# Kernel optimization log

Hardware: AMD Instinct MI355X
Metric: run time of the kernel (lower is better)

The kernel has to match this reference:

```python
import jax, jax.numpy as jnp
import numpy as np
from jax.ops import segment_sum


def gcn_conv(x, edge_index, W, b):
    """PyG GCNConv: add self-loops, symmetric D^-1/2 (A+I) D^-1/2 normalization,
    then aggregate normalized messages at target nodes. edge_weight=None -> ones."""
    N = x.shape[0]
    loops = jnp.arange(N, dtype=edge_index.dtype)
    row = jnp.concatenate([edge_index[0], loops])  # source nodes
    col = jnp.concatenate([edge_index[1], loops])  # target nodes
    w = jnp.ones(row.shape[0], dtype=x.dtype)
    deg = segment_sum(w, col, num_segments=N)
    dinv = jnp.where(deg > 0, jax.lax.rsqrt(deg), 0.0)
    norm = dinv[row] * dinv[col]                    # [E+N]
    xw = x @ W                                      # dense transform [N, out]
    msg = xw[row] * norm[:, None]                   # gather + scale [E+N, out]
    out = segment_sum(msg, col, num_segments=N)     # scatter-add at targets
    return out + b


def setup_inputs() -> dict:
    key = jax.random.key(0)
    k1, k2, k3, k4 = jax.random.split(key, 4)
    N, E, nhid, nfeat = 50000, 800000, 256, 128
    x = jax.random.normal(k1, (N, nhid), dtype=jnp.float32)
    edge_index = jax.random.randint(k2, (2, E), 0, N, dtype=jnp.int64)
    W1 = jax.random.normal(k3, (nhid, nhid), dtype=jnp.float32) * (1.0 / np.sqrt(nhid))
    b1 = jnp.zeros((nhid,), dtype=jnp.float32)
    W2 = jax.random.normal(k4, (nhid, nfeat), dtype=jnp.float32) * (1.0 / np.sqrt(nhid))
    b2 = jnp.zeros((nfeat,), dtype=jnp.float32)
    return {"x": x, "edge_index": edge_index, "W1": W1, "b1": b1, "W2": W2, "b2": b2}


def reference(x, edge_index, W1, b1, W2, b2):
    h = jax.nn.relu(gcn_conv(x, edge_index, W1, b1))
    # dropout is identity in eval mode (deterministic reference)
    return gcn_conv(h, edge_index, W2, b2)
```

## Files before the change

kernel.cpp:

```cpp
#include <hip/hip_runtime.h>
#include <math.h>


typedef _Float16 h8 __attribute__((ext_vector_type(8)));
typedef float    f32x4 __attribute__((ext_vector_type(4)));

#define CAP 64

__global__ void k_zero(int* __restrict__ deg, int* __restrict__ govf, int N) {
    int i = blockIdx.x * blockDim.x + threadIdx.x;
    if (i < N) deg[i] = 0;
    if (i == 0) *govf = 0;
}

__global__ __launch_bounds__(256) void k_count_prep(
    const int* __restrict__ col, int E, int* __restrict__ deg, int* __restrict__ rank,
    int ncb,
    const float* __restrict__ W1, const float* __restrict__ W2,
    _Float16* __restrict__ wt1, _Float16* __restrict__ wt2,
    int K, int n1, int n2)
{
    if ((int)blockIdx.x < ncb) {
        int i = blockIdx.x * blockDim.x + threadIdx.x;
        int s = ncb * blockDim.x;
        for (int e = i; e < E; e += s) rank[e] = atomicAdd(&deg[col[e]], 1);
        return;
    }
    int i = (blockIdx.x - ncb) * blockDim.x + threadIdx.x;
    int c1 = K * n1;
    if (i < c1) {
        int k = i / n1, n = i % n1;
        wt1[(long)n * K + k] = (_Float16)W1[i];
    } else if (i < c1 + K * n2) {
        int j = i - c1;
        int k = j / n2, n = j % n2;
        wt2[(long)n * K + k] = (_Float16)W2[j];
    }
}

__device__ __forceinline__ void gemm1_body(
    const float* __restrict__ X32, const _Float16* __restrict__ Wt,
    _Float16* __restrict__ Y, int M, int K, int by)
{
    __shared__ _Float16 As[128][40];
    __shared__ _Float16 Bs[256][40];

    const int bm = by * 128;
    const int tid = threadIdx.x;
    const int w = tid >> 6, l = tid & 63;
    const int wm = (w >> 2) * 64, wn = (w & 3) * 64;
    const int lr = l & 15, lg = l >> 4;

    const int arow = tid >> 2, acol = (tid & 3) * 8;
    const int brow = tid >> 1, bcol = (tid & 1) * 16;

    f32x4 acc[4][4];
    #pragma unroll
    for (int i = 0; i < 4; i++)
        #pragma unroll
        for (int j = 0; j < 4; j++)
            acc[i][j] = (f32x4){0.f, 0.f, 0.f, 0.f};

    float4 pf0, pf1;
    h8 pb0, pb1;

    auto loadA = [&](int k0) {
        int gm = bm + arow; if (gm >= M) gm = M - 1;
        pf0 = *reinterpret_cast<const float4*>(&X32[(long)gm * K + k0 + acol]);
        pf1 = *reinterpret_cast<const float4*>(&X32[(long)gm * K + k0 + acol + 4]);
    };
    auto loadB = [&](int k0) {
        pb0 = *reinterpret_cast<const h8*>(&Wt[(long)brow * K + k0 + bcol]);
        pb1 = *reinterpret_cast<const h8*>(&Wt[(long)brow * K + k0 + bcol + 8]);
    };

    loadA(0); loadB(0);
    for (int k0 = 0; k0 < K; k0 += 32) {
        h8 hv;
        hv[0] = (_Float16)pf0.x; hv[1] = (_Float16)pf0.y;
        hv[2] = (_Float16)pf0.z; hv[3] = (_Float16)pf0.w;
        hv[4] = (_Float16)pf1.x; hv[5] = (_Float16)pf1.y;
        hv[6] = (_Float16)pf1.z; hv[7] = (_Float16)pf1.w;
        *reinterpret_cast<h8*>(&As[arow][acol]) = hv;
        *reinterpret_cast<h8*>(&Bs[brow][bcol]) = pb0;
        *reinterpret_cast<h8*>(&Bs[brow][bcol + 8]) = pb1;
        __syncthreads();

        if (k0 + 32 < K) { loadA(k0 + 32); loadB(k0 + 32); }

        h8 a[4], b[4];
        #pragma unroll
        for (int i = 0; i < 4; i++)
            a[i] = *reinterpret_cast<const h8*>(&As[wm + i * 16 + lr][lg * 8]);
        #pragma unroll
        for (int j = 0; j < 4; j++)
            b[j] = *reinterpret_cast<const h8*>(&Bs[wn + j * 16 + lr][lg * 8]);
        #pragma unroll
        for (int i = 0; i < 4; i++)
            #pragma unroll
            for (int j = 0; j < 4; j++)
                acc[i][j] = __builtin_amdgcn_mfma_f32_16x16x32_f16(
                    a[i], b[j], acc[i][j], 0, 0, 0);
        __syncthreads();
    }

    #pragma unroll
    for (int i = 0; i < 4; i++) {
        #pragma unroll
        for (int r = 0; r < 4; r++) {
            int gm = bm + wm + i * 16 + lg * 4 + r;
            if (gm < M) {
                #pragma unroll
                for (int j = 0; j < 4; j++)
                    Y[(long)gm * 256 + wn + j * 16 + lr] =
                        (_Float16)acc[i][j][r];
            }
        }
    }
}

__global__ __launch_bounds__(512) void k_gemm_fill(
    const float* __restrict__ X32, const _Float16* __restrict__ Wt,
    _Float16* __restrict__ Y, int M, int K, int ngb,
    const int* __restrict__ row, const int* __restrict__ col,
    const int* __restrict__ rank, int E,
    const int* __restrict__ deg, float* __restrict__ dinv, int N,
    int* __restrict__ srcidx, int2* __restrict__ ovf, int* __restrict__ govf,
    int zb5)
{
    if ((int)blockIdx.x < ngb) {
        gemm1_body(X32, Wt, Y, M, K, blockIdx.x);
        return;
    }
    if ((int)blockIdx.x < ngb + zb5) {
        int i = (blockIdx.x - ngb) * blockDim.x + threadIdx.x;
        if (i < N) dinv[i] = rsqrtf(1.f + (float)deg[i]);
        return;
    }
    int g = (blockIdx.x - ngb - zb5) * blockDim.x + threadIdx.x;
    int nthreads = (gridDim.x - ngb - zb5) * blockDim.x;
    if ((E & 3) == 0) {
        int G4 = E >> 2;
        for (int q = g; q < G4; q += nthreads) {
            int e = q << 2;
            int4 c4 = *reinterpret_cast<const int4*>(&col[e]);
            int4 r4 = *reinterpret_cast<const int4*>(&row[e]);
            int4 k4 = *reinterpret_cast<const int4*>(&rank[e]);
            if (k4.x < CAP) srcidx[c4.x * CAP + k4.x] = r4.x;
            else { int o = atomicAdd(govf, 1); ovf[o] = make_int2(r4.x, c4.x); }
            if (k4.y < CAP) srcidx[c4.y * CAP + k4.y] = r4.y;
            else { int o = atomicAdd(govf, 1); ovf[o] = make_int2(r4.y, c4.y); }
            if (k4.z < CAP) srcidx[c4.z * CAP + k4.z] = r4.z;
            else { int o = atomicAdd(govf, 1); ovf[o] = make_int2(r4.z, c4.z); }
            if (k4.w < CAP) srcidx[c4.w * CAP + k4.w] = r4.w;
            else { int o = atomicAdd(govf, 1); ovf[o] = make_int2(r4.w, c4.w); }
        }
    } else {
        for (int e = g; e < E; e += nthreads) {
            int c = col[e], r = row[e], k = rank[e];
            if (k < CAP) srcidx[c * CAP + k] = r;
            else { int o = atomicAdd(govf, 1); ovf[o] = make_int2(r, c); }
        }
    }
}

__global__ __launch_bounds__(256) void k_gemm16(
    const _Float16* __restrict__ X16, const _Float16* __restrict__ Wt,
    _Float16* __restrict__ Y, int M, int K, int NC)
{
    __shared__ _Float16 As[128][40];
    __shared__ _Float16 Bs[128][40];

    const int bn = blockIdx.x * 128;
    const int bm = blockIdx.y * 128;
    const int tid = threadIdx.x;
    const int w = tid >> 6, l = tid & 63;
    const int wm = (w >> 1) * 64, wn = (w & 1) * 64;
    const int lr = l & 15, lg = l >> 4;
    const int xrow = tid >> 1, xcol = (tid & 1) * 16;

    f32x4 acc[4][4];
    #pragma unroll
    for (int i = 0; i < 4; i++)
        #pragma unroll
        for (int j = 0; j < 4; j++)
            acc[i][j] = (f32x4){0.f, 0.f, 0.f, 0.f};

    h8 pa0, pa1, pb0, pb1;
    auto loadA = [&](int k0) {
        int gm = bm + xrow; if (gm >= M) gm = M - 1;
        pa0 = *reinterpret_cast<const h8*>(&X16[(long)gm * K + k0 + xcol]);
        pa1 = *reinterpret_cast<const h8*>(&X16[(long)gm * K + k0 + xcol + 8]);
    };
    auto loadB = [&](int k0) {
        pb0 = *reinterpret_cast<const h8*>(&Wt[(long)(bn + xrow) * K + k0 + xcol]);
        pb1 = *reinterpret_cast<const h8*>(&Wt[(long)(bn + xrow) * K + k0 + xcol + 8]);
    };

    loadA(0); loadB(0);
    for (int k0 = 0; k0 < K; k0 += 32) {
        *reinterpret_cast<h8*>(&As[xrow][xcol]) = pa0;
        *reinterpret_cast<h8*>(&As[xrow][xcol + 8]) = pa1;
        *reinterpret_cast<h8*>(&Bs[xrow][xcol]) = pb0;
        *reinterpret_cast<h8*>(&Bs[xrow][xcol + 8]) = pb1;
        __syncthreads();

        if (k0 + 32 < K) { loadA(k0 + 32); loadB(k0 + 32); }

        h8 a[4], b[4];
        #pragma unroll
        for (int i = 0; i < 4; i++)
            a[i] = *reinterpret_cast<const h8*>(&As[wm + i * 16 + lr][lg * 8]);
        #pragma unroll
        for (int j = 0; j < 4; j++)
            b[j] = *reinterpret_cast<const h8*>(&Bs[wn + j * 16 + lr][lg * 8]);
        #pragma unroll
        for (int i = 0; i < 4; i++)
            #pragma unroll
            for (int j = 0; j < 4; j++)
                acc[i][j] = __builtin_amdgcn_mfma_f32_16x16x32_f16(
                    a[i], b[j], acc[i][j], 0, 0, 0);
        __syncthreads();
    }

    #pragma unroll
    for (int i = 0; i < 4; i++) {
        #pragma unroll
        for (int r = 0; r < 4; r++) {
            int gm = bm + wm + i * 16 + lg * 4 + r;
            if (gm < M) {
                #pragma unroll
                for (int j = 0; j < 4; j++)
                    Y[(long)gm * NC + bn + wn + j * 16 + lr] =
                        (_Float16)acc[i][j][r];
            }
        }
    }
}

template<bool F16OUT, bool RELU>
__global__ __launch_bounds__(256) void k_agg(
    const int* __restrict__ deg, const float* __restrict__ dinv,
    const int* __restrict__ srcidx,
    const int2* __restrict__ ovf, const int* __restrict__ govf,
    const _Float16* __restrict__ Y, const float* __restrict__ bias,
    int N, int FT, int fo,
    float* __restrict__ out32, _Float16* __restrict__ out16)
{
    int node = blockIdx.x * 4 + (threadIdx.x >> 6);
    if (node >= N) return;
    int lane = threadIdx.x & 63;
    int sub = lane >> 4;
    int fl  = lane & 15;
    const int fcol = fo + fl * 8;

    float dc = dinv[node];
    int cnt = min(deg[node], CAP);
    const int beg = node * CAP;

    float acc[8];
    if (sub == 0) {
        h8 v = *reinterpret_cast<const h8*>(&Y[(long)node * FT + fcol]);
        #pragma unroll
        for (int j = 0; j < 8; j++) acc[j] = dc * (float)v[j];
    } else {
        #pragma unroll
        for (int j = 0; j < 8; j++) acc[j] = 0.f;
    }

    int base16 = cnt & ~15;
    for (int i = sub * 4; i < base16; i += 16) {
        int4 r4 = *reinterpret_cast<const int4*>(&srcidx[beg + i]);
        float d0 = dinv[r4.x], d1 = dinv[r4.y], d2 = dinv[r4.z], d3 = dinv[r4.w];
        h8 v0 = *reinterpret_cast<const h8*>(&Y[(long)r4.x * FT + fcol]);
        h8 v1 = *reinterpret_cast<const h8*>(&Y[(long)r4.y * FT + fcol]);
        h8 v2 = *reinterpret_cast<const h8*>(&Y[(long)r4.z * FT + fcol]);
        h8 v3 = *reinterpret_cast<const h8*>(&Y[(long)r4.w * FT + fcol]);
        #pragma unroll
        for (int j = 0; j < 8; j++) {
            acc[j] = fmaf(d0, (float)v0[j], acc[j]);
            acc[j] = fmaf(d1, (float)v1[j], acc[j]);
            acc[j] = fmaf(d2, (float)v2[j], acc[j]);
            acc[j] = fmaf(d3, (float)v3[j], acc[j]);
        }
    }
    for (int i = base16 + sub; i < cnt; i += 4) {
        int r = srcidx[beg + i];
        float d = dinv[r];
        h8 v = *reinterpret_cast<const h8*>(&Y[(long)r * FT + fcol]);
        #pragma unroll
        for (int j = 0; j < 8; j++) acc[j] = fmaf(d, (float)v[j], acc[j]);
    }
    {
        int no = *govf;
        for (int t = sub; t < no; t += 4) {
            int2 pr = ovf[t];
            if (pr.y == node) {
                float d = dinv[pr.x];
                h8 v = *reinterpret_cast<const h8*>(&Y[(long)pr.x * FT + fcol]);
                #pragma unroll
                for (int j = 0; j < 8; j++) acc[j] = fmaf(d, (float)v[j], acc[j]);
            }
        }
    }

    #pragma unroll
    for (int m = 16; m < 64; m <<= 1)
        #pragma unroll
        for (int j = 0; j < 8; j++)
            acc[j] += __shfl_xor(acc[j], m, 64);

    const float4* b4 = reinterpret_cast<const float4*>(&bias[fcol]);
    float4 blo = b4[0], bhi = b4[1];
    float r8[8];
    r8[0] = fmaf(dc, acc[0], blo.x); r8[1] = fmaf(dc, acc[1], blo.y);
    r8[2] = fmaf(dc, acc[2], blo.z); r8[3] = fmaf(dc, acc[3], blo.w);
    r8[4] = fmaf(dc, acc[4], bhi.x); r8[5] = fmaf(dc, acc[5], bhi.y);
    r8[6] = fmaf(dc, acc[6], bhi.z); r8[7] = fmaf(dc, acc[7], bhi.w);
    if (RELU) {
        #pragma unroll
        for (int j = 0; j < 8; j++) r8[j] = fmaxf(r8[j], 0.f);
    }

    long base = (long)node * FT + fcol;
    if (F16OUT) {
        if (sub == 0) {
            h8 o;
            #pragma unroll
            for (int j = 0; j < 8; j++) o[j] = (_Float16)r8[j];
            *reinterpret_cast<h8*>(&out16[base]) = o;
        }
    } else {
        if (sub == 0) {
            *reinterpret_cast<float4*>(&out32[base]) =
                make_float4(r8[0], r8[1], r8[2], r8[3]);
        } else if (sub == 1) {
            *reinterpret_cast<float4*>(&out32[base + 4]) =
                make_float4(r8[4], r8[5], r8[6], r8[7]);
        }
    }
}

extern "C" void kernel_launch(void* const* d_in, const int* in_sizes, int n_in,
                              void* d_out, int out_size, void* d_ws, size_t ws_size,
                              hipStream_t stream)
{
    const float* x   = (const float*)d_in[0];
    const int*   ei  = (const int*)d_in[1];
    const float* W1  = (const float*)d_in[2];
    const float* b1  = (const float*)d_in[3];
    const float* W2  = (const float*)d_in[4];
    const float* b2  = (const float*)d_in[5];

    const int nhid  = in_sizes[3];
    const int nfeat = in_sizes[5];
    const int N     = in_sizes[0] / nhid;
    const int E     = in_sizes[1] / 2;

    const int* row = ei;
    const int* col = ei + E;

    size_t cur = 0;
    auto alloc = [&](size_t bytes) {
        void* p = (char*)d_ws + cur;
        cur += (bytes + 255) & ~(size_t)255;
        return p;
    };
    int*       deg_i  = (int*)alloc((size_t)N * 4);
    int*       govf   = (int*)alloc(256);
    float*     dinv   = (float*)alloc((size_t)N * 4);
    int*       rank   = (int*)alloc((size_t)E * 4);
    int*       srcidx = (int*)alloc((size_t)N * CAP * 4);
    int2*      ovf    = (int2*)alloc((size_t)E * 8);
    _Float16*  wt1    = (_Float16*)alloc((size_t)nhid * nhid * 2);
    _Float16*  wt2    = (_Float16*)alloc((size_t)nhid * nfeat * 2);
    _Float16*  y16    = (_Float16*)alloc((size_t)N * nhid * 2);
    _Float16*  h16    = (_Float16*)alloc((size_t)N * nhid * 2);
    _Float16*  y2     = (_Float16*)alloc((size_t)N * nfeat * 2);
    float*     out    = (float*)d_out;
    (void)ws_size; (void)n_in; (void)out_size;

    const int T = 256;
    const int zb  = (N + T - 1) / T;
    const int zb5 = (N + 511) / 512;
    const int gy  = (N + 127) / 128;

    k_zero<<<zb, T, 0, stream>>>(deg_i, govf, N);

    {
        const int ncb = 1024;
        int pb = (nhid * (nhid + nfeat) + T - 1) / T;
        k_count_prep<<<ncb + pb, T, 0, stream>>>(
            col, E, deg_i, rank, ncb, W1, W2, wt1, wt2, nhid, nhid, nfeat);
    }

    {
        int ngb = gy;
        k_gemm_fill<<<ngb + zb5 + 1024, 512, 0, stream>>>(
            x, wt1, y16, N, nhid, ngb,
            row, col, rank, E, deg_i, dinv, N, srcidx, ovf, govf, zb5);
    }

    {
        int nblk = (N + 3) / 4;
        k_agg<true, true><<<nblk, T, 0, stream>>>(
            deg_i, dinv, srcidx, ovf, govf, y16, b1, N, nhid, 0, nullptr, h16);
        k_agg<true, true><<<nblk, T, 0, stream>>>(
            deg_i, dinv, srcidx, ovf, govf, y16, b1, N, nhid, 128, nullptr, h16);
    }

    {
        dim3 grid(nfeat / 128, (N + 127) / 128);
        k_gemm16<<<grid, T, 0, stream>>>(h16, wt2, y2, N, nhid, nfeat);
    }
    {
        int nblk = (N + 3) / 4;
        k_agg<false, false><<<nblk, T, 0, stream>>>(
            deg_i, dinv, srcidx, ovf, govf, y2, b2, N, nfeat, 0, out, nullptr);
    }
}
```

Baseline: 177.0 us.

## Shrink neighbor cap, split layer-2 aggregation by column halves, regroup prep kernels

Lowers the per-node neighbor slot capacity from 64 to 32, which shrinks the srcidx buffer and sends more edges to the overflow list. The aggregation kernel gains a lanes-per-row template parameter so layer 2 runs as two 64-column passes with 8 lanes per row, and each wave processes more neighbors in parallel. The weight transpose moves into the zeroing kernel and edge counting becomes its own kernel. Risks: with mean degree about 16, more nodes exceed 32 neighbors, so the linearly scanned overflow list grows, and every node pays for scanning it.

```diff
diff --git a/kernel.cpp b/kernel.cpp
--- a/kernel.cpp
+++ b/kernel.cpp
@@ -5,37 +5,37 @@
 typedef _Float16 h8 __attribute__((ext_vector_type(8)));
 typedef float    f32x4 __attribute__((ext_vector_type(4)));
 
-#define CAP 64
-
-__global__ void k_zero(int* __restrict__ deg, int* __restrict__ govf, int N) {
+#define CAP 32
+
+__global__ void k_zero_prep(int* __restrict__ deg, int* __restrict__ govf, int N,
+                            const float* __restrict__ W1, const float* __restrict__ W2,
+                            _Float16* __restrict__ wt1, _Float16* __restrict__ wt2,
+                            int K, int n1, int n2, int zb)
+{
+    if ((int)blockIdx.x < zb) {
+        int i = blockIdx.x * blockDim.x + threadIdx.x;
+        if (i < N) deg[i] = 0;
+        if (i == 0) *govf = 0;
+    } else {
+        int i = (blockIdx.x - zb) * blockDim.x + threadIdx.x;
+        int c1 = K * n1;
+        if (i < c1) {
+            int k = i / n1, n = i % n1;
+            wt1[(long)n * K + k] = (_Float16)W1[i];
+        } else if (i < c1 + K * n2) {
+            int j = i - c1;
+            int k = j / n2, n = j % n2;
+            wt2[(long)n * K + k] = (_Float16)W2[j];
+        }
+    }
+}
+
+__global__ __launch_bounds__(256) void k_count(
+    const int* __restrict__ col, int E, int* __restrict__ deg, int* __restrict__ rank)
+{
     int i = blockIdx.x * blockDim.x + threadIdx.x;
-    if (i < N) deg[i] = 0;
-    if (i == 0) *govf = 0;
-}
-
-__global__ __launch_bounds__(256) void k_count_prep(
-    const int* __restrict__ col, int E, int* __restrict__ deg, int* __restrict__ rank,
-    int ncb,
-    const float* __restrict__ W1, const float* __restrict__ W2,
-    _Float16* __restrict__ wt1, _Float16* __restrict__ wt2,
-    int K, int n1, int n2)
-{
-    if ((int)blockIdx.x < ncb) {
-        int i = blockIdx.x * blockDim.x + threadIdx.x;
-        int s = ncb * blockDim.x;
-        for (int e = i; e < E; e += s) rank[e] = atomicAdd(&deg[col[e]], 1);
-        return;
-    }
-    int i = (blockIdx.x - ncb) * blockDim.x + threadIdx.x;
-    int c1 = K * n1;
-    if (i < c1) {
-        int k = i / n1, n = i % n1;
-        wt1[(long)n * K + k] = (_Float16)W1[i];
-    } else if (i < c1 + K * n2) {
-        int j = i - c1;
-        int k = j / n2, n = j % n2;
-        wt2[(long)n * K + k] = (_Float16)W2[j];
-    }
+    int s = gridDim.x * blockDim.x;
+    for (int e = i; e < E; e += s) rank[e] = atomicAdd(&deg[col[e]], 1);
 }
 
 __device__ __forceinline__ void gemm1_body(
@@ -238,7 +238,7 @@
     }
 }
 
-template<bool F16OUT, bool RELU>
+template<int LPR, bool F16OUT, bool RELU>
 __global__ __launch_bounds__(256) void k_agg(
     const int* __restrict__ deg, const float* __restrict__ dinv,
     const int* __restrict__ srcidx,
@@ -247,11 +247,13 @@
     int N, int FT, int fo,
     float* __restrict__ out32, _Float16* __restrict__ out16)
 {
+    const int G = 64 / LPR;
+    const int STEP = 4 * G;
     int node = blockIdx.x * 4 + (threadIdx.x >> 6);
     if (node >= N) return;
     int lane = threadIdx.x & 63;
-    int sub = lane >> 4;
-    int fl  = lane & 15;
+    int sub = lane / LPR;
+    int fl  = lane % LPR;
     const int fcol = fo + fl * 8;
 
     float dc = dinv[node];
@@ -268,8 +270,8 @@
         for (int j = 0; j < 8; j++) acc[j] = 0.f;
     }
 
-    int base16 = cnt & ~15;
-    for (int i = sub * 4; i < base16; i += 16) {
+    int basea = cnt & ~(STEP - 1);
+    for (int i = sub * 4; i < basea; i += STEP) {
         int4 r4 = *reinterpret_cast<const int4*>(&srcidx[beg + i]);
         float d0 = dinv[r4.x], d1 = dinv[r4.y], d2 = dinv[r4.z], d3 = dinv[r4.w];
         h8 v0 = *reinterpret_cast<const h8*>(&Y[(long)r4.x * FT + fcol]);
@@ -284,7 +286,7 @@
             acc[j] = fmaf(d3, (float)v3[j], acc[j]);
         }
     }
-    for (int i = base16 + sub; i < cnt; i += 4) {
+    for (int i = basea + sub; i < cnt; i += G) {
         int r = srcidx[beg + i];
         float d = dinv[r];
         h8 v = *reinterpret_cast<const h8*>(&Y[(long)r * FT + fcol]);
@@ -293,7 +295,7 @@
     }
     {
         int no = *govf;
-        for (int t = sub; t < no; t += 4) {
+        for (int t = sub; t < no; t += G) {
             int2 pr = ovf[t];
             if (pr.y == node) {
                 float d = dinv[pr.x];
@@ -305,7 +307,7 @@
     }
 
     #pragma unroll
-    for (int m = 16; m < 64; m <<= 1)
+    for (int m = LPR; m < 64; m <<= 1)
         #pragma unroll
         for (int j = 0; j < 8; j++)
             acc[j] += __shfl_xor(acc[j], m, 64);
@@ -385,14 +387,13 @@
     const int zb5 = (N + 511) / 512;
     const int gy  = (N + 127) / 128;
 
-    k_zero<<<zb, T, 0, stream>>>(deg_i, govf, N);
-
-    {
-        const int ncb = 1024;
+    {
         int pb = (nhid * (nhid + nfeat) + T - 1) / T;
-        k_count_prep<<<ncb + pb, T, 0, stream>>>(
-            col, E, deg_i, rank, ncb, W1, W2, wt1, wt2, nhid, nhid, nfeat);
-    }
+        k_zero_prep<<<zb + pb, T, 0, stream>>>(deg_i, govf, N, W1, W2, wt1, wt2,
+                                               nhid, nhid, nfeat, zb);
+    }
+
+    k_count<<<2048, T, 0, stream>>>(col, E, deg_i, rank);
 
     {
         int ngb = gy;
@@ -403,9 +404,9 @@
 
     {
         int nblk = (N + 3) / 4;
-        k_agg<true, true><<<nblk, T, 0, stream>>>(
+        k_agg<16, true, true><<<nblk, T, 0, stream>>>(
             deg_i, dinv, srcidx, ovf, govf, y16, b1, N, nhid, 0, nullptr, h16);
-        k_agg<true, true><<<nblk, T, 0, stream>>>(
+        k_agg<16, true, true><<<nblk, T, 0, stream>>>(
             deg_i, dinv, srcidx, ovf, govf, y16, b1, N, nhid, 128, nullptr, h16);
     }
 
@@ -415,7 +416,9 @@
     }
     {
         int nblk = (N + 3) / 4;
-        k_agg<false, false><<<nblk, T, 0, stream>>>(
+        k_agg<8, false, false><<<nblk, T, 0, stream>>>(
             deg_i, dinv, srcidx, ovf, govf, y2, b2, N, nfeat, 0, out, nullptr);
-    }
-}
+        k_agg<8, false, false><<<nblk, T, 0, stream>>>(
+            deg_i, dinv, srcidx, ovf, govf, y2, b2, N, nfeat, 64, out, nullptr);
+    }
+}
```

Result: slower. 215.3 us (+21.7%).

## Fuse layer-1 aggregation, bias and ReLU into the layer-2 GEMM

Applied to the files above, without the earlier changes.

Replaces the two layer-1 aggregation launches and the separate layer-2 GEMM with one kernel. Each 64-row block gathers neighbor rows of Y1 for one K-slice, applies normalization, bias and ReLU, writes the result into the GEMM A tile in shared memory, and then runs MFMA against W2. This removes the h16 intermediate write and read and two launches. In exchange, the gather is done per 32-wide K slice with 8-half (16-byte) loads per thread and no prefetch of the next tile, which may lower memory efficiency. The overflow path also rescans the whole overflow list in every block for every K slice.

```diff
diff --git a/kernel.cpp b/kernel.cpp
--- a/kernel.cpp
+++ b/kernel.cpp
@@ -5,11 +5,12 @@
 typedef _Float16 h8 __attribute__((ext_vector_type(8)));
 typedef float    f32x4 __attribute__((ext_vector_type(4)));
 
-#define CAP 64
-
-__global__ void k_zero(int* __restrict__ deg, int* __restrict__ govf, int N) {
+#define CAP  64
+#define CAPP 68
+
+__global__ void k_zero(int* __restrict__ deg, int* __restrict__ govf, int N64) {
     int i = blockIdx.x * blockDim.x + threadIdx.x;
-    if (i < N) deg[i] = 0;
+    if (i < N64) deg[i] = 0;
     if (i == 0) *govf = 0;
 }
 
@@ -164,74 +165,156 @@
     }
 }
 
-__global__ __launch_bounds__(256) void k_gemm16(
-    const _Float16* __restrict__ X16, const _Float16* __restrict__ Wt,
-    _Float16* __restrict__ Y, int M, int K, int NC)
-{
-    __shared__ _Float16 As[128][40];
+__global__ __launch_bounds__(256) void k_hgemm(
+    const _Float16* __restrict__ Y1, const _Float16* __restrict__ Wt2,
+    const float* __restrict__ b1,
+    const int* __restrict__ deg, const float* __restrict__ dinv,
+    const int* __restrict__ srcidx,
+    const int2* __restrict__ ovf, const int* __restrict__ govf,
+    _Float16* __restrict__ Y2, int N, int K, int NC2)
+{
+    __shared__ _Float16 As[64][40];
     __shared__ _Float16 Bs[128][40];
-
-    const int bn = blockIdx.x * 128;
-    const int bm = blockIdx.y * 128;
+    __shared__ int   slots[64 * CAPP];
+    __shared__ float sdv[64 * CAPP];
+    __shared__ float sdinv[64];
+    __shared__ int   sdeg[64];
+
+    const int bm = blockIdx.x * 64;
     const int tid = threadIdx.x;
     const int w = tid >> 6, l = tid & 63;
-    const int wm = (w >> 1) * 64, wn = (w & 1) * 64;
+    const int wm = (w >> 1) * 32, wn = (w & 1) * 64;
     const int lr = l & 15, lg = l >> 4;
-    const int xrow = tid >> 1, xcol = (tid & 1) * 16;
-
-    f32x4 acc[4][4];
+
+    {
+        const int4* s4 = reinterpret_cast<const int4*>(srcidx);
+        for (int q = tid; q < 64 * (CAP / 4); q += 256) {
+            int r = q >> 4, i4 = q & 15;
+            int4 v = s4[(long)(bm + r) * (CAP / 4) + i4];
+            *reinterpret_cast<int4*>(&slots[r * CAPP + i4 * 4]) = v;
+        }
+        if (tid < 64) {
+            int n = bm + tid;
+            sdeg[tid]  = (n < N) ? min(deg[n], CAP) : 0;
+            sdinv[tid] = (n < N) ? dinv[n] : 0.f;
+        }
+    }
+    __syncthreads();
+    for (int idx = tid; idx < 64 * CAP; idx += 256) {
+        int r = idx >> 6, i = idx & 63;
+        if (i < sdeg[r]) sdv[r * CAPP + i] = dinv[slots[r * CAPP + i]];
+    }
+    __syncthreads();
+
+    const int arow = tid >> 2, af = (tid & 3) * 8;
+    const int brow = tid >> 1, bf = (tid & 1) * 16;
+    const int n = bm + arow;
+    const bool valid = n < N;
+    const float dc = sdinv[arow];
+    const int cnt = sdeg[arow];
+    const int novf = *govf;
+
+    f32x4 acc[2][4];
     #pragma unroll
-    for (int i = 0; i < 4; i++)
+    for (int i = 0; i < 2; i++)
         #pragma unroll
         for (int j = 0; j < 4; j++)
             acc[i][j] = (f32x4){0.f, 0.f, 0.f, 0.f};
 
-    h8 pa0, pa1, pb0, pb1;
-    auto loadA = [&](int k0) {
-        int gm = bm + xrow; if (gm >= M) gm = M - 1;
-        pa0 = *reinterpret_cast<const h8*>(&X16[(long)gm * K + k0 + xcol]);
-        pa1 = *reinterpret_cast<const h8*>(&X16[(long)gm * K + k0 + xcol + 8]);
-    };
-    auto loadB = [&](int k0) {
-        pb0 = *reinterpret_cast<const h8*>(&Wt[(long)(bn + xrow) * K + k0 + xcol]);
-        pb1 = *reinterpret_cast<const h8*>(&Wt[(long)(bn + xrow) * K + k0 + xcol + 8]);
-    };
-
-    loadA(0); loadB(0);
     for (int k0 = 0; k0 < K; k0 += 32) {
-        *reinterpret_cast<h8*>(&As[xrow][xcol]) = pa0;
-        *reinterpret_cast<h8*>(&As[xrow][xcol + 8]) = pa1;
-        *reinterpret_cast<h8*>(&Bs[xrow][xcol]) = pb0;
-        *reinterpret_cast<h8*>(&Bs[xrow][xcol + 8]) = pb1;
+        float a8[8];
+        if (valid) {
+            h8 v = *reinterpret_cast<const h8*>(&Y1[(long)n * K + k0 + af]);
+            #pragma unroll
+            for (int j = 0; j < 8; j++) a8[j] = dc * (float)v[j];
+        } else {
+            #pragma unroll
+            for (int j = 0; j < 8; j++) a8[j] = 0.f;
+        }
+        int i = 0;
+        for (; i + 4 <= cnt; i += 4) {
+            int r0 = slots[arow * CAPP + i + 0];
+            int r1 = slots[arow * CAPP + i + 1];
+            int r2 = slots[arow * CAPP + i + 2];
+            int r3 = slots[arow * CAPP + i + 3];
+            float d0 = sdv[arow * CAPP + i + 0];
+            float d1 = sdv[arow * CAPP + i + 1];
+            float d2 = sdv[arow * CAPP + i + 2];
+            float d3 = sdv[arow * CAPP + i + 3];
+            h8 v0 = *reinterpret_cast<const h8*>(&Y1[(long)r0 * K + k0 + af]);
+            h8 v1 = *reinterpret_cast<const h8*>(&Y1[(long)r1 * K + k0 + af]);
+            h8 v2 = *reinterpret_cast<const h8*>(&Y1[(long)r2 * K + k0 + af]);
+            h8 v3 = *reinterpret_cast<const h8*>(&Y1[(long)r3 * K + k0 + af]);
+            #pragma unroll
+            for (int j = 0; j < 8; j++) {
+                a8[j] = fmaf(d0, (float)v0[j], a8[j]);
+                a8[j] = fmaf(d1, (float)v1[j], a8[j]);
+                a8[j] = fmaf(d2, (float)v2[j], a8[j]);
+                a8[j] = fmaf(d3, (float)v3[j], a8[j]);
+            }
+        }
+        for (; i < cnt; i++) {
+            int r = slots[arow * CAPP + i];
+            float d = sdv[arow * CAPP + i];
+            h8 v = *reinterpret_cast<const h8*>(&Y1[(long)r * K + k0 + af]);
+            #pragma unroll
+            for (int j = 0; j < 8; j++) a8[j] = fmaf(d, (float)v[j], a8[j]);
+        }
+        if (novf) {
+            for (int t = 0; t < novf; t++) {
+                int2 pr = ovf[t];
+                if (pr.y == n) {
+                    float d = dinv[pr.x];
+                    h8 v = *reinterpret_cast<const h8*>(&Y1[(long)pr.x * K + k0 + af]);
+                    #pragma unroll
+                    for (int j = 0; j < 8; j++) a8[j] = fmaf(d, (float)v[j], a8[j]);
+                }
+            }
+        }
+        {
+            float4 bl0 = *reinterpret_cast<const float4*>(&b1[k0 + af]);
+            float4 bl1 = *reinterpret_cast<const float4*>(&b1[k0 + af + 4]);
+            float hb[8];
+            hb[0] = fmaf(dc, a8[0], bl0.x); hb[1] = fmaf(dc, a8[1], bl0.y);
+            hb[2] = fmaf(dc, a8[2], bl0.z); hb[3] = fmaf(dc, a8[3], bl0.w);
+            hb[4] = fmaf(dc, a8[4], bl1.x); hb[5] = fmaf(dc, a8[5], bl1.y);
+            hb[6] = fmaf(dc, a8[6], bl1.z); hb[7] = fmaf(dc, a8[7], bl1.w);
+            h8 hv;
+            #pragma unroll
+            for (int j = 0; j < 8; j++) hv[j] = (_Float16)fmaxf(hb[j], 0.f);
+            *reinterpret_cast<h8*>(&As[arow][af]) = hv;
+        }
+        *reinterpret_cast<h8*>(&Bs[brow][bf]) =
+            *reinterpret_cast<const h8*>(&Wt2[(long)brow * K + k0 + bf]);
+        *reinterpret_cast<h8*>(&Bs[brow][bf + 8]) =
+            *reinterpret_cast<const h8*>(&Wt2[(long)brow * K + k0 + bf + 8]);
         __syncthreads();
 
-        if (k0 + 32 < K) { loadA(k0 + 32); loadB(k0 + 32); }
-
-        h8 a[4], b[4];
-        #pragma unroll
-        for (int i = 0; i < 4; i++)
-            a[i] = *reinterpret_cast<const h8*>(&As[wm + i * 16 + lr][lg * 8]);
+        h8 a[2], b[4];
+        #pragma unroll
+        for (int i2 = 0; i2 < 2; i2++)
+            a[i2] = *reinterpret_cast<const h8*>(&As[wm + i2 * 16 + lr][lg * 8]);
         #pragma unroll
         for (int j = 0; j < 4; j++)
             b[j] = *reinterpret_cast<const h8*>(&Bs[wn + j * 16 + lr][lg * 8]);
         #pragma unroll
-        for (int i = 0; i < 4; i++)
+        for (int i2 = 0; i2 < 2; i2++)
             #pragma unroll
             for (int j = 0; j < 4; j++)
-                acc[i][j] = __builtin_amdgcn_mfma_f32_16x16x32_f16(
-                    a[i], b[j], acc[i][j], 0, 0, 0);
+                acc[i2][j] = __builtin_amdgcn_mfma_f32_16x16x32_f16(
+                    a[i2], b[j], acc[i2][j], 0, 0, 0);
         __syncthreads();
     }
 
     #pragma unroll
-    for (int i = 0; i < 4; i++) {
+    for (int i = 0; i < 2; i++) {
         #pragma unroll
         for (int r = 0; r < 4; r++) {
             int gm = bm + wm + i * 16 + lg * 4 + r;
-            if (gm < M) {
+            if (gm < N) {
                 #pragma unroll
                 for (int j = 0; j < 4; j++)
-                    Y[(long)gm * NC + bn + wn + j * 16 + lr] =
+                    Y2[(long)gm * NC2 + wn + j * 16 + lr] =
                         (_Float16)acc[i][j][r];
             }
         }
@@ -356,6 +439,7 @@
     const int nfeat = in_sizes[5];
     const int N     = in_sizes[0] / nhid;
     const int E     = in_sizes[1] / 2;
+    const int N64   = (N + 63) & ~63;
 
     const int* row = ei;
     const int* col = ei + E;
@@ -366,26 +450,26 @@
         cur += (bytes + 255) & ~(size_t)255;
         return p;
     };
-    int*       deg_i  = (int*)alloc((size_t)N * 4);
+    int*       deg_i  = (int*)alloc((size_t)N64 * 4);
     int*       govf   = (int*)alloc(256);
-    float*     dinv   = (float*)alloc((size_t)N * 4);
+    float*     dinv   = (float*)alloc((size_t)N64 * 4);
     int*       rank   = (int*)alloc((size_t)E * 4);
-    int*       srcidx = (int*)alloc((size_t)N * CAP * 4);
+    int*       srcidx = (int*)alloc((size_t)N64 * CAP * 4);
     int2*      ovf    = (int2*)alloc((size_t)E * 8);
     _Float16*  wt1    = (_Float16*)alloc((size_t)nhid * nhid * 2);
     _Float16*  wt2    = (_Float16*)alloc((size_t)nhid * nfeat * 2);
     _Float16*  y16    = (_Float16*)alloc((size_t)N * nhid * 2);
-    _Float16*  h16    = (_Float16*)alloc((size_t)N * nhid * 2);
     _Float16*  y2     = (_Float16*)alloc((size_t)N * nfeat * 2);
     float*     out    = (float*)d_out;
     (void)ws_size; (void)n_in; (void)out_size;
 
     const int T = 256;
-    const int zb  = (N + T - 1) / T;
+    const int zb  = (N64 + T - 1) / T;
     const int zb5 = (N + 511) / 512;
     const int gy  = (N + 127) / 128;
-
-    k_zero<<<zb, T, 0, stream>>>(deg_i, govf, N);
+    const int gy2 = (N + 63) / 64;
+
+    k_zero<<<zb, T, 0, stream>>>(deg_i, govf, N64);
 
     {
         const int ncb = 1024;
@@ -401,18 +485,9 @@
             row, col, rank, E, deg_i, dinv, N, srcidx, ovf, govf, zb5);
     }
 
-    {
-        int nblk = (N + 3) / 4;
-        k_agg<true, true><<<nblk, T, 0, stream>>>(
-            deg_i, dinv, srcidx, ovf, govf, y16, b1, N, nhid, 0, nullptr, h16);
-        k_agg<true, true><<<nblk, T, 0, stream>>>(
-            deg_i, dinv, srcidx, ovf, govf, y16, b1, N, nhid, 128, nullptr, h16);
-    }
-
-    {
-        dim3 grid(nfeat / 128, (N + 127) / 128);
-        k_gemm16<<<grid, T, 0, stream>>>(h16, wt2, y2, N, nhid, nfeat);
-    }
+    k_hgemm<<<gy2, T, 0, stream>>>(
+        y16, wt2, b1, deg_i, dinv, srcidx, ovf, govf, y2, N, nhid, nfeat);
+
     {
         int nblk = (N + 3) / 4;
         k_agg<false, false><<<nblk, T, 0, stream>>>(
```

New measurement: 207.0 us. +17.0%, slower.
